# Optimization experiments

Hardware: AMD Instinct MI355X
Metric: run time of the kernel (lower is better)

## Reference

```python
import jax, jax.numpy as jnp
import numpy as np

R_MAX = 5.0
P_CUT = 5
NAVG = 16.0
L_OF_LM = np.array([0, 1, 1, 1, 2, 2, 2, 2, 2, 3, 3, 3, 3, 3, 3, 3])


def _sph(v):
    # real spherical harmonics up to l=3 on normalized vectors, [E,16]
    n = jnp.sqrt(jnp.sum(v * v, -1, keepdims=True) + 1e-12)
    u = v / n
    x, y, z = u[..., 0], u[..., 1], u[..., 2]
    s3, s15, s5 = np.sqrt(3.0), np.sqrt(15.0), np.sqrt(5.0)
    s70, s105, s42, s7 = np.sqrt(70.0), np.sqrt(105.0), np.sqrt(42.0), np.sqrt(7.0)
    Y = [jnp.ones_like(x),
         s3 * x, s3 * y, s3 * z,
         s15 * x * y, s15 * y * z, 0.5 * s5 * (3 * z * z - 1.0), s15 * x * z, 0.5 * s15 * (x * x - y * y),
         0.25 * s70 * y * (3 * x * x - y * y), s105 * x * y * z, 0.25 * s42 * y * (5 * z * z - 1.0),
         0.5 * s7 * z * (5 * z * z - 3.0), 0.25 * s42 * x * (5 * z * z - 1.0),
         0.5 * s105 * z * (x * x - y * y), 0.25 * s70 * x * (3 * x * x - y * y)]
    return jnp.stack(Y, -1)


def _radial(r):
    # Bessel basis * smooth polynomial cutoff, r: [E] -> [E, 8]
    n = jnp.arange(1, 9, dtype=r.dtype)
    bess = np.sqrt(2.0 / R_MAX) * jnp.sin(n * np.pi * r[:, None] / R_MAX) / (r[:, None] + 1e-9)
    u = r / R_MAX
    p = float(P_CUT)
    f = 1.0 - 0.5 * (p + 1) * (p + 2) * u ** P_CUT + p * (p + 2) * u ** (P_CUT + 1) - 0.5 * p * (p + 1) * u ** (P_CUT + 2)
    f = jnp.where(u < 1.0, f, 0.0)
    return bess * f[:, None]


def _energy(node_attrs, positions, shifts, atomic_energies, W_embed, W_up, W_r1, W_r2, W_r3,
            W_lin, W_skip, U1, U2, U3, Wc1, Wc2, Wc3, W_prod, W_readout,
            edge_index, batch, num_graphs):
    send, recv = edge_index[0], edge_index[1]
    vec = positions[recv] - positions[send] + shifts
    r = jnp.sqrt(jnp.sum(vec * vec, -1) + 1e-12)
    Y = _sph(vec)                       # [E,16]
    edge_feats = _radial(r)             # [E,8]
    h = node_attrs @ W_embed            # [N,K] scalar node features
    lidx = jnp.asarray(L_OF_LM)
    N = h.shape[0]
    for i in range(2):
        h_up = h @ W_up[i]
        w = jax.nn.silu(edge_feats @ W_r1[i])
        w = jax.nn.silu(w @ W_r2[i])
        w = (w @ W_r3[i]).reshape(edge_feats.shape[0], -1, 4)   # [E,K,4] per-l radial tp weights
        w_lm = w[:, :, lidx]                                    # [E,K,16]
        m = w_lm * h_up[send][:, :, None] * Y[:, None, :]       # scalar x SH tensor product messages
        agg = jax.ops.segment_sum(m, recv, num_segments=N) / NAVG
        Wm = W_lin[i][lidx]                                     # [16,K,K] per-l linear
        mixed = jnp.einsum('nkm,mkh->nhm', agg, Wm)
        sc = jnp.einsum('nk,ne,ekh->nh', h, node_attrs, W_skip[i])  # element-wise skip tp -> scalars
        A = mixed.at[:, :, 0].add(sc)                           # [N,K,16] A-basis
        # ACE symmetric product basis (invariant outputs), element-dependent weights
        w1 = jnp.einsum('ne,epk->npk', node_attrs, Wc1[i])
        b1 = jnp.einsum('nkp,npk->nk', jnp.einsum('nka,ap->nkp', A, U1), w1)
        AA = jnp.einsum('nka,nkb->nkab', A, A)                  # [N,K,16,16]
        w2 = jnp.einsum('ne,epk->npk', node_attrs, Wc2[i])
        b2 = jnp.einsum('nkp,npk->nk', jnp.einsum('nkab,abp->nkp', AA, U2), w2)
        T3 = jnp.einsum('nkab,abcp->nkcp', AA, U3)              # [N,K,16,8]
        w3 = jnp.einsum('ne,epk->npk', node_attrs, Wc3[i])
        b3 = jnp.einsum('nkp,npk->nk', jnp.einsum('nkcp,nkc->nkp', T3, A), w3)
        h = (b1 + b2 + b3) @ W_prod[i]
    node_es = h @ W_readout                                     # [N]
    node_e0 = node_attrs @ atomic_energies
    e0 = jax.ops.segment_sum(node_e0, batch, num_segments=num_graphs)
    inter = jax.ops.segment_sum(node_es, batch, num_segments=num_graphs)
    return e0 + inter


def setup_inputs():
    key = jax.random.key(0)
    ks = jax.random.split(key, 24)
    N, E, K, NE, G, NB = 2048, 32768, 128, 10, 16, 8
    P1, P2, P3, L = 2, 4, 8, 16

    def rn(k, shape, fan):
        return jax.random.normal(k, shape, jnp.float32) / np.sqrt(fan)

    elem = jax.random.randint(ks[0], (N,), 0, NE)
    return {
        'node_attrs': jax.nn.one_hot(elem, NE, dtype=jnp.float32),
        'positions': jax.random.uniform(ks[1], (N, 3), jnp.float32) * 6.0,
        'shifts': jnp.zeros((E, 3), jnp.float32),
        'atomic_energies': jax.random.normal(ks[2], (NE,), jnp.float32),
        'W_embed': rn(ks[3], (NE, K), NE),
        'W_up': rn(ks[4], (2, K, K), K),
        'W_r1': rn(ks[5], (2, NB, 64), NB),
        'W_r2': rn(ks[6], (2, 64, 64), 64),
        'W_r3': rn(ks[7], (2, 64, K * 4), 64),
        'W_lin': rn(ks[8], (2, 4, K, K), K),
        'W_skip': rn(ks[9], (2, NE, K, K), K),
        'U1': rn(ks[10], (L, P1), L),
        'U2': rn(ks[11], (L, L, P2), L * L),
        'U3': rn(ks[12], (L, L, L, P3), L * L * L),
        'Wc1': rn(ks[13], (2, NE, P1, K), P1),
        'Wc2': rn(ks[14], (2, NE, P2, K), P2),
        'Wc3': rn(ks[15], (2, NE, P3, K), P3),
        'W_prod': rn(ks[16], (2, K, K), K),
        'W_readout': rn(ks[17], (K,), K),
        'edge_index': jax.random.randint(ks[18], (2, E), 0, N).astype(jnp.int32),
        'batch': jnp.sort(jax.random.randint(ks[19], (N,), 0, G)).astype(jnp.int32),
        'num_graphs': 16,
    }


def reference(node_attrs, positions, shifts, atomic_energies, W_embed, W_up, W_r1, W_r2, W_r3,
              W_lin, W_skip, U1, U2, U3, Wc1, Wc2, Wc3, W_prod, W_readout,
              edge_index, batch, num_graphs):
    e_fn = lambda pos: _energy(node_attrs, pos, shifts, atomic_energies, W_embed, W_up, W_r1, W_r2,
                               W_r3, W_lin, W_skip, U1, U2, U3, Wc1, Wc2, Wc3, W_prod, W_readout,
                               edge_index, batch, num_graphs)
    energy = e_fn(positions)
    forces = -jax.grad(lambda p: e_fn(p).sum())(positions)
    return energy, forces
```

## Files before the change

### kernel.cpp

```cpp
#include <hip/hip_runtime.h>
#include <math.h>

#define KCH 128
#define NELEM 10
#define NPAIR 136
#define PSZ   2176

__device__ __forceinline__ int lidxf(int m){ return (m==0)?0:((m<4)?1:((m<9)?2:3)); }
__device__ __forceinline__ float siluf(float z){ return z/(1.f+expf(-z)); }
__device__ __forceinline__ float dsiluf(float z){ float s=1.f/(1.f+expf(-z)); return s*(1.f+z*(1.f-s)); }

__global__ void k_zero(float* p, int n){
  int i = blockIdx.x*256 + threadIdx.x;
  if(i<n) p[i]=0.f;
}

__global__ void k_elem(const float* attrs, int* elem, int N){
  int n = blockIdx.x*256 + threadIdx.x;
  if(n>=N) return;
  int z=0;
  for(int e=0;e<NELEM;++e) if(attrs[n*NELEM+e] > 0.5f) z=e;
  elem[n]=z;
}

// ... 209 lines not shown
  int e0 = blockIdx.x*16;
  for(int it=0; it<4; ++it){
    int item = t + it*256;
    int el = item>>6, j = item&63;
    float z=0;
    if(e0+el < E){
      const float* efe = ef + (size_t)(e0+el)*8;
      #pragma unroll
      for(int b=0;b<8;++b) z += efe[b]*Wr1[b*64+j];
    }
    t1s[el][j] = siluf(z);
  }
  __syncthreads();
  for(int it=0; it<4; ++it){
    int item = t + it*256;
    int el = item>>6, j = item&63;
    float z=0;
    #pragma unroll
    for(int i=0;i<64;++i) z += t1s[el][i]*Wr2[i*64+j];
    t2s[el][j] = siluf(z);
  }
  __syncthreads();
  float a0[16], a1[16];
  #pragma unroll
  for(int el=0;el<16;++el){ a0[el]=0.f; a1[el]=0.f; }
  for(int j=0;j<64;++j){
    float wa = Wr3[j*512 + t];
    float wb = Wr3[j*512 + t + 256];
    #pragma unroll
    for(int el=0;el<16;++el){
      float tv = t2s[el][j];
      a0[el] += tv*wa;
      a1[el] += tv*wb;
    }
  }
  for(int el=0;el<16;++el){
    if(e0+el < E){
      w[(size_t)(e0+el)*512 + t] = a0[el];
      w[(size_t)(e0+el)*512 + t + 256] = a1[el];
    }
  }
}

__global__ __launch_bounds__(256) void k_gather(const float* hup, const float* w, const float* Y,
                                                const int* rptr, const int* snds,
                                                float* agg, int E){
  int n = blockIdx.x;
  int t = threadIdx.x;
  int k = t & 127, mg = t >> 7;
  float acc[8] = {0,0,0,0,0,0,0,0};
  int s0 = rptr[n], s1 = rptr[n+1];
  for(int i=s0;i<s1;++i){
    int snd = snds[i];
    float hv = hup[(size_t)snd*KCH + k];
    float4 w4 = ((const float4*)(w + (size_t)i*512))[k];
    const float* Ye = Y + (size_t)i*16 + mg*8;
    if(mg==0){
      acc[0] += w4.x*hv*Ye[0];
      acc[1] += w4.y*hv*Ye[1];
      acc[2] += w4.y*hv*Ye[2];
      acc[3] += w4.y*hv*Ye[3];
      acc[4] += w4.z*hv*Ye[4];
      acc[5] += w4.z*hv*Ye[5];
      acc[6] += w4.z*hv*Ye[6];
      acc[7] += w4.z*hv*Ye[7];
    } else {
      acc[0] += w4.z*hv*Ye[0];
      acc[1] += w4.w*hv*Ye[1];
      acc[2] += w4.w*hv*Ye[2];
      acc[3] += w4.w*hv*Ye[3];
      acc[4] += w4.w*hv*Ye[4];
      acc[5] += w4.w*hv*Ye[5];
      acc[6] += w4.w*hv*Ye[6];
      acc[7] += w4.w*hv*Ye[7];
    }
  }
  const float inv = 1.f/16.f;
  float* ap = agg + (size_t)n*2048 + k*16 + mg*8;
  #pragma unroll
  for(int j=0;j<8;++j) ap[j] = acc[j]*inv;
}

__global__ __launch_bounds__(256) void k_mixed2(const float* X, const float* hin, const int* elem,
                                                const float* Wb, const float* Wsk,
                                                float* Out, float* gh, int N, int mode){
  __shared__ float xs[4][2048];
  __shared__ float hs[4][128];
  __shared__ int zs[4];
  int t = threadIdx.x;
  int n0 = blockIdx.x*4;
  for(int q=0;q<4;++q){
    const float4* Xp = (const float4*)(X + (size_t)(n0+q)*2048);
    float4* Xs = (float4*)xs[q];
    Xs[t] = Xp[t]; Xs[t+256] = Xp[t+256];
  }
  if(mode==0 && t<128){
    for(int q=0;q<4;++q) hs[q][t] = hin[(size_t)(n0+q)*KCH + t];
  }
  if(t<4) zs[t]=elem[n0+t];
  __syncthreads();
  int kg = t&31, mg=(t>>5)&3, half=t>>7;
  int k0 = kg*4, m0 = mg*4;
  int q0 = half*2, q1=q0+1;
  float acc0[4][4], acc1[4][4];
  #pragma unroll
  for(int a=0;a<4;++a){
    #pragma unroll
    for(int b=0;b<4;++b){acc0[a][b]=0.f;acc1[a][b]=0.f;}
  }
  for(int s=0;s<KCH;++s){
    float4 x0 = *(const float4*)&xs[q0][s*16+m0];
    float4 x1 = *(const float4*)&xs[q1][s*16+m0];
    #pragma unroll
    for(int mj=0;mj<4;++mj){
      const float4 wv = *(const float4*)&Wb[(size_t)(m0+mj)*16384 + s*128 + k0];
      float xm0 = (mj==0)?x0.x:((mj==1)?x0.y:((mj==2)?x0.z:x0.w));
      float xm1 = (mj==0)?x1.x:((mj==1)?x1.y:((mj==2)?x1.z:x1.w));
      acc0[mj][0]+=xm0*wv.x; acc0[mj][1]+=xm0*wv.y; acc0[mj][2]+=xm0*wv.z; acc0[mj][3]+=xm0*wv.w;
      acc1[mj][0]+=xm1*wv.x; acc1[mj][1]+=xm1*wv.y; acc1[mj][2]+=xm1*wv.z; acc1[mj][3]+=xm1*wv.w;
    }
  }
  if(mode==0 && mg==0){
    const float* W0 = Wsk + (size_t)zs[q0]*16384;
    const float* W1 = Wsk + (size_t)zs[q1]*16384;
    for(int s=0;s<KCH;++s){
      float h0v=hs[q0][s], h1v=hs[q1][s];
      float4 w0 = *(const float4*)&W0[s*128+k0];
      float4 w1 = *(const float4*)&W1[s*128+k0];
      acc0[0][0]+=h0v*w0.x; acc0[0][1]+=h0v*w0.y; acc0[0][2]+=h0v*w0.z; acc0[0][3]+=h0v*w0.w;
      acc1[0][0]+=h1v*w1.x; acc1[0][1]+=h1v*w1.y; acc1[0][2]+=h1v*w1.z; acc1[0][3]+=h1v*w1.w;
    }
  }
  #pragma unroll
  for(int ki=0;ki<4;++ki){
    *(float4*)&Out[(size_t)(n0+q0)*2048 + (k0+ki)*16 + m0] = make_float4(acc0[0][ki],acc0[1][ki],acc0[2][ki],acc0[3][ki]);
    *(float4*)&Out[(size_t)(n0+q1)*2048 + (k0+ki)*16 + m0] = make_float4(acc1[0][ki],acc1[1][ki],acc1[2][ki],acc1[3][ki]);
  }
  if(mode==2 && mg==0){
    const float* W0 = Wsk + (size_t)zs[q0]*16384;
    const float* W1 = Wsk + (size_t)zs[q1]*16384;
    float a0[4]={0,0,0,0}, a1[4]={0,0,0,0};
    for(int s=0;s<KCH;++s){
      float x0v = xs[q0][s*16], x1v = xs[q1][s*16];
      float4 w0 = *(const float4*)&W0[s*128+k0];
      float4 w1 = *(const float4*)&W1[s*128+k0];
      a0[0]+=x0v*w0.x; a0[1]+=x0v*w0.y; a0[2]+=x0v*w0.z; a0[3]+=x0v*w0.w;
      a1[0]+=x1v*w1.x; a1[1]+=x1v*w1.y; a1[2]+=x1v*w1.z; a1[3]+=x1v*w1.w;
    }
    *(float4*)&gh[(size_t)(n0+q0)*KCH + k0] = make_float4(a0[0],a0[1],a0[2],a0[3]);
    *(float4*)&gh[(size_t)(n0+q1)*KCH + k0] = make_float4(a1[0],a1[1],a1[2],a1[3]);
  }
}

__global__ __launch_bounds__(256) void k_poly_fwd(const float* A, const float* C1, const float* C2S, const float* P,
                                                  const int* eptr, const int* eidx, float* B){
  __shared__ float Ps[PSZ];
  __shared__ float C2s_[256];
  __shared__ float C1s_[16];
  int t = threadIdx.x;
  int z = blockIdx.x >> 7, c = blockIdx.x & 127;
  size_t cb = (size_t)z*KCH + c;
  for(int i=t;i<PSZ;i+=256) Ps[i] = P[cb*PSZ + i];
  if(t<256) C2s_[t] = C2S[cb*256 + t];
  if(t<16) C1s_[t] = C1[cb*16 + t];
  __syncthreads();
  int s0 = eptr[z], cnt = eptr[z+1]-s0;
  for(int idx=t; idx<cnt; idx+=256){
    int n = eidx[s0+idx];
    float a[16];
    const float4* ap = (const float4*)(A + (size_t)n*2048 + c*16);
    float4 a4;
    a4=ap[0]; a[0]=a4.x;a[1]=a4.y;a[2]=a4.z;a[3]=a4.w;
    a4=ap[1]; a[4]=a4.x;a[5]=a4.y;a[6]=a4.z;a[7]=a4.w;
    a4=ap[2]; a[8]=a4.x;a[9]=a4.y;a[10]=a4.z;a[11]=a4.w;
    a4=ap[3]; a[12]=a4.x;a[13]=a4.y;a[14]=a4.z;a[15]=a4.w;
    float G[16];
    #pragma unroll
    for(int x=0;x<16;++x) G[x]=0.f;
    int pair=0;
    #pragma unroll
    for(int j=0;j<16;++j){
      #pragma unroll
      for(int k=j;k<16;++k){
        float pp = a[j]*a[k];
        const float* Pp = &Ps[pair*16];
        #pragma unroll
        for(int x=0;x<16;++x) G[x] += pp*Pp[x];
        ++pair;
      }
    }
    float b1=0;
    #pragma unroll
    for(int i=0;i<16;++i) b1 += a[i]*C1s_[i];
    float b2=0;
    for(int i=0;i<16;++i){
      float s=0;
      #pragma unroll
      for(int j=0;j<16;++j) s += a[j]*C2s_[i*16+j];
      b2 += a[i]*s;
    }
    float b3o=0;
    #pragma unroll
    for(int x=0;x<16;++x) b3o += a[x]*G[x];
    B[(size_t)n*KCH + c] = b1 + 0.5f*b2 + b3o*(1.f/3.f);
  }
}

__global__ __launch_bounds__(256) void k_poly_bwd(const float* A, const float* C1, const float* C2S, const float* P,
                                                  const int* eptr, const int* eidx,
                                                  const float* gBvec, const float* gBbuf, float* gA){
  __shared__ float Ps[PSZ];
  __shared__ float C2s_[256];
  __shared__ float C1s_[16];
  int t = threadIdx.x;
  int z = blockIdx.x >> 7, c = blockIdx.x & 127;
  size_t cb = (size_t)z*KCH + c;
  for(int i=t;i<PSZ;i+=256) Ps[i] = P[cb*PSZ + i];
  if(t<256) C2s_[t] = C2S[cb*256 + t];
  if(t<16) C1s_[t] = C1[cb*16 + t];
  __syncthreads();
  int s0 = eptr[z], cnt = eptr[z+1]-s0;
  for(int idx=t; idx<cnt; idx+=256){
    int n = eidx[s0+idx];
    float a[16];
    const float4* ap = (const float4*)(A + (size_t)n*2048 + c*16);
    float4 a4;
    a4=ap[0]; a[0]=a4.x;a[1]=a4.y;a[2]=a4.z;a[3]=a4.w;
    a4=ap[1]; a[4]=a4.x;a[5]=a4.y;a[6]=a4.z;a[7]=a4.w;
    a4=ap[2]; a[8]=a4.x;a[9]=a4.y;a[10]=a4.z;a[11]=a4.w;
    a4=ap[3]; a[12]=a4.x;a[13]=a4.y;a[14]=a4.z;a[15]=a4.w;
    float gB = gBvec ? gBvec[c] : gBbuf[(size_t)n*KCH + c];
    float G[16];
    #pragma unroll
    for(int x=0;x<16;++x) G[x]=C1s_[x];
    for(int x=0;x<16;++x){
      float s=0;
      #pragma unroll
      for(int b=0;b<16;++b) s += a[b]*C2s_[x*16+b];
      G[x]+=s;
    }
    int pair=0;
    #pragma unroll
    for(int j=0;j<16;++j){
      #pragma unroll
      for(int k=j;k<16;++k){
        float pp = a[j]*a[k];
        const float* Pp = &Ps[pair*16];
        #pragma unroll
        for(int x=0;x<16;++x) G[x] += pp*Pp[x];
        ++pair;
      }
    }
    float* gp = gA + (size_t)n*2048 + c*16;
    #pragma unroll
    for(int x=0;x<16;++x) gp[x] = gB*G[x];
  }
}

__global__ __launch_bounds__(256) void k_edge_gw(const float* gagg, const float* hup, const float* w,
                                                 const float* Y, const float* dY,
                                                 const int* snds, const int* rcvs, int E,
                                                 float* gw, float* ghup, float* gvec, int do_ghup, int accv){
  __shared__ float Ys[2][16];
  __shared__ float gYp[2][2][16];
  int t = threadIdx.x;
  int le = t>>7, k = t&127;
  int e = blockIdx.x*2 + le;
  const float inv16 = 1.f/16.f;
  if(t<32){ int l2=t>>4; int ec=blockIdx.x*2+l2; if(ec<E) Ys[l2][t&15] = Y[(size_t)ec*16 + (t&15)]; }
  __syncthreads();
  bool valid = (e<E);
  int eC = valid ? e : (E-1);
  int snd = snds[eC], rcv = rcvs[eC];
  float hv = hup[(size_t)snd*KCH + k];
  float4 w4 = ((const float4*)(w + (size_t)eC*512))[k];
  float g[16];
  const float4* gp = (const float4*)(gagg + (size_t)rcv*2048 + k*16);
  float4 v4;
  v4=gp[0]; g[0]=v4.x;g[1]=v4.y;g[2]=v4.z;g[3]=v4.w;
  v4=gp[1]; g[4]=v4.x;g[5]=v4.y;g[6]=v4.z;g[7]=v4.w;
  v4=gp[2]; g[8]=v4.x;g[9]=v4.y;g[10]=v4.z;g[11]=v4.w;
  v4=gp[3]; g[12]=v4.x;g[13]=v4.y;g[14]=v4.z;g[15]=v4.w;
  const float* Yl = Ys[le];
  float p0 = g[0]*Yl[0];
  float p1 = g[1]*Yl[1]+g[2]*Yl[2]+g[3]*Yl[3];
  float p2 = g[4]*Yl[4]+g[5]*Yl[5]+g[6]*Yl[6]+g[7]*Yl[7]+g[8]*Yl[8];
  float p3 = g[9]*Yl[9]+g[10]*Yl[10]+g[11]*Yl[11]+g[12]*Yl[12]+g[13]*Yl[13]+g[14]*Yl[14]+g[15]*Yl[15];
  float hs = hv*inv16;
  ((float4*)(gw + (size_t)eC*512))[k] = make_float4(p0*hs, p1*hs, p2*hs, p3*hs);
  if(do_ghup && valid){
    float s = (p0*w4.x + p1*w4.y + p2*w4.z + p3*w4.w)*inv16;
    atomicAdd(&ghup[(size_t)snd*KCH+k], s);
  }
  float q[16];
  q[0]=g[0]*w4.x*hv;
  q[1]=g[1]*w4.y*hv; q[2]=g[2]*w4.y*hv; q[3]=g[3]*w4.y*hv;
  q[4]=g[4]*w4.z*hv; q[5]=g[5]*w4.z*hv; q[6]=g[6]*w4.z*hv; q[7]=g[7]*w4.z*hv; q[8]=g[8]*w4.z*hv;
  #pragma unroll
  for(int m=9;m<16;++m) q[m]=g[m]*w4.w*hv;
  #pragma unroll
  for(int m=0;m<16;++m){
    float vv=q[m];
    #pragma unroll
    for(int off2=1; off2<64; off2<<=1) vv += __shfl_xor(vv, off2, 64);
    q[m]=vv;
  }
  if((t&63)==0){
    int wv2 = (t>>6)&1;
    #pragma unroll
    for(int m=0;m<16;++m) gYp[le][wv2][m]=q[m];
  }
  __syncthreads();
  if(t<6){
    int le2 = t/3, jj = t-le2*3;
    int ee = blockIdx.x*2 + le2;
    if(ee<E){
      float s=0;
      #pragma unroll
      for(int m=0;m<16;++m)
        s += (gYp[le2][0][m]+gYp[le2][1][m])*inv16 * dY[(size_t)ee*48 + m*3 + jj];
      if(accv) gvec[(size_t)ee*3+jj] += s;
      else     gvec[(size_t)ee*3+jj]  = s;
    }
  }
}

__global__ __launch_bounds__(256) void k_radial_bwd2(const float* gw, const float* ef, const float* defdr,
                                                     const float* vec, const float* rr,
                                                     const float* Wr1, const float* Wr2,
                                                     const float* Wr2T, const float* Wr3T,
                                                     float* gvec, int E){
  __shared__ float t1s[16][64];
  __shared__ float gz2s[16][64];
  __shared__ float efS[16][8];
  __shared__ float defS[16][8];
  int t = threadIdx.x;
  int e0 = blockIdx.x*16;
  int j = t&63, g = t>>6;
  if(t<128){ int el=t>>3, b=t&7; int ec=e0+el;
    if(ec<E){ efS[el][b]=ef[(size_t)ec*8+b]; defS[el][b]=defdr[(size_t)ec*8+b]; }
    else { efS[el][b]=0.f; defS[el][b]=0.f; } }
  __syncthreads();
  float ds1[4], ds2[4];
  #pragma unroll
  for(int q=0;q<4;++q){
    int el = g*4+q;
    float z=0;
    #pragma unroll
    for(int b=0;b<8;++b) z += efS[el][b]*Wr1[b*64+j];
    t1s[el][j]=siluf(z); ds1[q]=dsiluf(z);
  }
  __syncthreads();
  float gt2[4]={0,0,0,0};
  #pragma unroll
  for(int q=0;q<4;++q){
    int el = g*4+q;
    float z=0;
    for(int i=0;i<64;++i) z += t1s[el][i]*Wr2[i*64+j];
    ds2[q]=dsiluf(z);
  }
  for(int i4=0;i4<128;++i4){
    float wv0 = Wr3T[(i4*4+0)*64+j];
    float wv1 = Wr3T[(i4*4+1)*64+j];
    float wv2 = Wr3T[(i4*4+2)*64+j];
    float wv3 = Wr3T[(i4*4+3)*64+j];
    #pragma unroll
    for(int q=0;q<4;++q){
      int ec = e0 + g*4 + q; if(ec>=E) ec=E-1;
      const float4 g4 = *(const float4*)(gw + (size_t)ec*512 + i4*4);
      gt2[q] += g4.x*wv0 + g4.y*wv1 + g4.z*wv2 + g4.w*wv3;
    }
  }
  #pragma unroll
  for(int q=0;q<4;++q) gz2s[g*4+q][j] = gt2[q]*ds2[q];
  __syncthreads();
  #pragma unroll
  for(int q=0;q<4;++q){
    int el = g*4+q;
    float s=0;
    for(int o=0;o<64;++o) s += gz2s[el][o]*Wr2T[o*64+j];
    float gz1 = s*ds1[q];
    float cj=0;
    #pragma unroll
    for(int b=0;b<8;++b) cj += Wr1[b*64+j]*defS[el][b];
    float p = gz1*cj;
    #pragma unroll
    for(int off2=1;off2<64;off2<<=1) p += __shfl_xor(p,off2,64);
    int ec = e0+el;
    if(j<3 && ec<E)
      gvec[(size_t)ec*3+j] += p * vec[(size_t)ec*3+j] / rr[ec];
  }
}

__global__ __launch_bounds__(256) void k_edge_bwd2(const float* gagg, const float* hup, const float* w,
                                                   const float* Y, const float* dY,
                                                   const float* vec, const float* rr,
                                                   const float* ef, const float* defdr,
                                                   const float* Wr1, const float* Wr2,
                                                   const float* Wr2T, const float* Wr3T,
                                                   const int* snds, const int* rcvs, int E,
                                                   float* ghup, float* gvec, int do_ghup, int accv){
  __shared__ float Ys[4][16];
  __shared__ float gwS[4][512];
  __shared__ float gYp[4][2][16];
  __shared__ float t1s[4][64];
  __shared__ float gz2s[4][64];
  __shared__ float efS[4][8];
  __shared__ float defS[4][8];
  int t = threadIdx.x;
  int e0 = blockIdx.x*4;
  const float inv16 = 1.f/16.f;
  if(t<64){ int le=t>>4; int ec = e0+le; if(ec<E) Ys[le][t&15] = Y[(size_t)ec*16 + (t&15)]; }
  else if(t<96){ int i=t-64; int le=i>>3; int ec=e0+le; if(ec<E) efS[le][i&7]=ef[(size_t)ec*8+(i&7)]; }
  else if(t<128){ int i=t-96; int le=i>>3; int ec=e0+le; if(ec<E) defS[le][i&7]=defdr[(size_t)ec*8+(i&7)]; }
  __syncthreads();
  for(int rep=0;rep<2;++rep){
    int le = (t>>7) + 2*rep;
    int k = t&127;
    int e = e0+le;
    bool valid = (e<E);
    int eC = valid ? e : (E-1);
    int snd = snds[eC], rcv = rcvs[eC];
    float hv = hup[(size_t)snd*KCH + k];
    float4 w4 = ((const float4*)(w + (size_t)eC*512))[k];
    float g[16];
    const float4* gp = (const float4*)(gagg + (size_t)rcv*2048 + k*16);
    float4 v4;
    v4=gp[0]; g[0]=v4.x;g[1]=v4.y;g[2]=v4.z;g[3]=v4.w;
    v4=gp[1]; g[4]=v4.x;g[5]=v4.y;g[6]=v4.z;g[7]=v4.w;
    v4=gp[2]; g[8]=v4.x;g[9]=v4.y;g[10]=v4.z;g[11]=v4.w;
    v4=gp[3]; g[12]=v4.x;g[13]=v4.y;g[14]=v4.z;g[15]=v4.w;
    const float* Yl = Ys[le];
    float p0 = g[0]*Yl[0];
    float p1 = g[1]*Yl[1]+g[2]*Yl[2]+g[3]*Yl[3];
    float p2 = g[4]*Yl[4]+g[5]*Yl[5]+g[6]*Yl[6]+g[7]*Yl[7]+g[8]*Yl[8];
    float p3 = g[9]*Yl[9]+g[10]*Yl[10]+g[11]*Yl[11]+g[12]*Yl[12]+g[13]*Yl[13]+g[14]*Yl[14]+g[15]*Yl[15];
    float hs = hv*inv16;
    ((float4*)(&gwS[le][k*4]))[0] = make_float4(p0*hs, p1*hs, p2*hs, p3*hs);
    if(do_ghup && valid){
      float s = (p0*w4.x + p1*w4.y + p2*w4.z + p3*w4.w)*inv16;
      atomicAdd(&ghup[(size_t)snd*KCH+k], s);
    }
    float q[16];
    q[0]=g[0]*w4.x*hv;
    q[1]=g[1]*w4.y*hv; q[2]=g[2]*w4.y*hv; q[3]=g[3]*w4.y*hv;
    q[4]=g[4]*w4.z*hv; q[5]=g[5]*w4.z*hv; q[6]=g[6]*w4.z*hv; q[7]=g[7]*w4.z*hv; q[8]=g[8]*w4.z*hv;
    #pragma unroll
    for(int m=9;m<16;++m) q[m]=g[m]*w4.w*hv;
    #pragma unroll
    for(int m=0;m<16;++m){
      float vv=q[m];
      #pragma unroll
      for(int off2=1; off2<64; off2<<=1) vv += __shfl_xor(vv, off2, 64);
      q[m]=vv;
    }
    if((t&63)==0){
      int wv2 = (t>>6)&1;
      #pragma unroll
      for(int m=0;m<16;++m) gYp[le][wv2][m]=q[m];
    }
  }
  __syncthreads();
  {
    int el = t>>6, j = t&63;
    int e = e0+el;
    bool valid = (e<E);
    int eC = valid ? e : (E-1);
    float z1=0;
    #pragma unroll
    for(int b=0;b<8;++b) z1 += efS[el][b]*Wr1[b*64+j];
    float ds1v = dsiluf(z1);
    t1s[el][j] = siluf(z1);
    __syncthreads();
    float z2=0;
    for(int i=0;i<64;++i) z2 += t1s[el][i]*Wr2[i*64+j];
    float ds2v = dsiluf(z2);
    float gt2=0;
    for(int i=0;i<512;++i) gt2 += gwS[el][i]*Wr3T[i*64+j];
    gz2s[el][j] = gt2*ds2v;
    __syncthreads();
    float gz1=0;
    for(int o=0;o<64;++o) gz1 += gz2s[el][o]*Wr2T[o*64+j];
    gz1 *= ds1v;
    float cj=0;
    #pragma unroll
    for(int b=0;b<8;++b) cj += Wr1[b*64+j]*defS[el][b];
    float p = gz1*cj;
    #pragma unroll
    for(int off2=1;off2<64;off2<<=1) p += __shfl_xor(p,off2,64);
    if(j<3 && valid){
      float s = p * vec[(size_t)eC*3+j] / rr[eC];
      #pragma unroll
      for(int m=0;m<16;++m)
        s += (gYp[el][0][m]+gYp[el][1][m])*inv16 * dY[(size_t)eC*48 + m*3 + j];
      if(accv) gvec[(size_t)eC*3+j] += s;
      else     gvec[(size_t)eC*3+j]  = s;
    }
  }
}

__global__ void k_energy(const float* h2, const float* Wro, const float* AE,
                         const int* elem, const int* batch, float* out, int N){
  int n = blockIdx.x*256 + threadIdx.x;
  if(n>=N) return;
  float s=0;
  for(int k=0;k<KCH;++k) s += h2[(size_t)n*KCH+k]*Wro[k];
  s += AE[elem[n]];
  atomicAdd(&out[batch[n]], s);
}

__global__ void k_forces(const float* gvec, const int* snds, const int* rcvs, int E, float* fout){
  int i = blockIdx.x*256 + threadIdx.x;
  if(i>=E*3) return;
  int e = i/3, j = i - e*3;
  float g = gvec[i];
  atomicAdd(&fout[(size_t)snds[e]*3+j], g);
  atomicAdd(&fout[(size_t)rcvs[e]*3+j], -g);
}

extern "C" void kernel_launch(void* const* d_in, const int* in_sizes, int n_in,
                              void* d_out, int out_size, void* d_ws, size_t ws_size,
                              hipStream_t stream){
  const float* attrs  = (const float*)d_in[0];
  const float* pos    = (const float*)d_in[1];
  const float* shifts = (const float*)d_in[2];
  const float* AE     = (const float*)d_in[3];
  const float* Wemb   = (const float*)d_in[4];
  const float* Wup    = (const float*)d_in[5];
  const float* Wr1    = (const float*)d_in[6];
  const float* Wr2    = (const float*)d_in[7];
  const float* Wr3    = (const float*)d_in[8];
  const float* Wlin   = (const float*)d_in[9];
  const float* Wskip  = (const float*)d_in[10];
  const float* U1     = (const float*)d_in[11];
  const float* U2     = (const float*)d_in[12];
  const float* U3     = (const float*)d_in[13];
  const float* Wc1    = (const float*)d_in[14];
  const float* Wc2    = (const float*)d_in[15];
  const float* Wc3    = (const float*)d_in[16];
  const float* Wprod  = (const float*)d_in[17];
  const float* Wro    = (const float*)d_in[18];
  const int*   ei     = (const int*)d_in[19];
  const int*   batch  = (const int*)d_in[20];
  int N = in_sizes[1]/3;
  int E = in_sizes[19]/2;
  float* out = (float*)d_out;
  int G = out_size - 3*N;

  char* base = (char*)d_ws;
  size_t off = 0;
  auto alloc = [&](size_t nbytes)->void*{
    void* p = base + off;
    off += (nbytes + 255) & ~(size_t)255;
    return p;
  };
  int* elem = (int*)alloc((size_t)N*4);
  int* rptr = (int*)alloc((size_t)(N+1)*4);
  int* rcnt = (int*)alloc((size_t)N*4);
  int* rcur = (int*)alloc((size_t)N*4);
  int* ecnt = (int*)alloc((size_t)NELEM*4);
  int* ecur = (int*)alloc((size_t)NELEM*4);
  size_t zspan = (size_t)((base+off) - (char*)rcnt) / 4;
  int* ridx = (int*)alloc((size_t)E*4);
  int* eptr = (int*)alloc((size_t)(NELEM+1)*4);
  int* eidx = (int*)alloc((size_t)N*4);
  int* snds = (int*)alloc((size_t)E*4);
  int* rcvs = (int*)alloc((size_t)E*4);
  float* h0   = (float*)alloc((size_t)N*KCH*4);
  float* h1   = (float*)alloc((size_t)N*KCH*4);
  float* h2   = (float*)alloc((size_t)N*KCH*4);
  float* hup0 = (float*)alloc((size_t)N*KCH*4);
  float* hup1 = (float*)alloc((size_t)N*KCH*4);
  float* vecb = (float*)alloc((size_t)E*3*4);
  float* rb   = (float*)alloc((size_t)E*4);
  float* Yb   = (float*)alloc((size_t)E*16*4);
  float* dYb  = (float*)alloc((size_t)E*48*4);
  float* efb  = (float*)alloc((size_t)E*8*4);
  float* defb = (float*)alloc((size_t)E*8*4);
  float* wb   = (float*)alloc((size_t)E*512*4);
  float* A0   = (float*)alloc((size_t)N*2048*4);
  float* A1   = (float*)alloc((size_t)N*2048*4);
  float* aggb = (float*)alloc((size_t)N*2048*4);
  float* gAb  = (float*)alloc((size_t)N*2048*4);
  float* Bbuf = (float*)alloc((size_t)N*KCH*4);
  float* gh1  = (float*)alloc((size_t)N*KCH*4);
  float* ghup = (float*)alloc((size_t)N*KCH*4);
  float* gB0b = (float*)alloc((size_t)N*KCH*4);
  float* gB1v = (float*)alloc((size_t)KCH*4);
  float* gvecb= (float*)alloc((size_t)E*3*4);
  float* C1b  = (float*)alloc((size_t)NELEM*KCH*16*4);
  float* C2Sb = (float*)alloc((size_t)NELEM*KCH*256*4);
  float* Pb   = (float*)alloc((size_t)NELEM*KCH*PSZ*4);
  float* U2s  = (float*)alloc(1024*4);
  float* U3s  = (float*)alloc(32768*4);
  float* WupT1   = (float*)alloc(16384*4);
  float* WprodT0 = (float*)alloc(16384*4);
  float* WskipT1 = (float*)alloc((size_t)NELEM*16384*4);
  float* Wbig0  = (float*)alloc((size_t)16*16384*4);
  float* Wbig1  = (float*)alloc((size_t)16*16384*4);
  float* WbigT0 = (float*)alloc((size_t)16*16384*4);
  float* WbigT1 = (float*)alloc((size_t)16*16384*4);
  float* Wr3T0   = (float*)alloc(32768*4);
  float* Wr3T1   = (float*)alloc(32768*4);
  float* Wr2T0   = (float*)alloc(4096*4);
  float* Wr2T1   = (float*)alloc(4096*4);
  if(off > ws_size) return;
  float* wb1 = wb; int have_wb1 = 0;
  if(off + (size_t)E*512*4 <= ws_size){ wb1 = (float*)alloc((size_t)E*512*4); have_wb1 = 1; }
  float *C1_1=C1b, *C2_1=C2Sb, *P_1=Pb; int have_c2 = 0;
  {
    size_t need = ((size_t)NELEM*KCH*16 + (size_t)NELEM*KCH*256 + (size_t)NELEM*KCH*PSZ)*4 + 1024;
    if(off + need <= ws_size){
      C1_1 = (float*)alloc((size_t)NELEM*KCH*16*4);
      C2_1 = (float*)alloc((size_t)NELEM*KCH*256*4);
      P_1  = (float*)alloc((size_t)NELEM*KCH*PSZ*4);
      have_c2 = 1;
    }
  }
  float* gwb = nullptr; int have_gw = 0;
  if(off + (size_t)E*512*4 <= ws_size){ gwb = (float*)alloc((size_t)E*512*4); have_gw = 1; }

  const int KK = KCH*KCH;
  dim3 b256(256), b128(128);
  #define GR(n) dim3(((n)+255)/256)

  k_zero<<<GR(out_size),b256,0,stream>>>(out, out_size);
  k_zero<<<GR((int)zspan),b256,0,stream>>>((float*)rcnt, (int)zspan);
  k_zero<<<GR(N*KCH),b256,0,stream>>>(ghup, N*KCH);

  k_elem<<<GR(N),b256,0,stream>>>(attrs, elem, N);
  k_h0<<<GR(N*KCH),b256,0,stream>>>(Wemb, elem, h0, N);

  k_hist<<<GR(E),b256,0,stream>>>(ei+E, rcnt, E);
  k_scan<<<1,b256,0,stream>>>(rcnt, rptr, N);
  k_scatter<<<GR(E),b256,0,stream>>>(ei+E, rptr, rcur, ridx, E);
  k_hist<<<GR(N),b256,0,stream>>>(elem, ecnt, N);
  k_scan<<<1,b256,0,stream>>>(ecnt, eptr, NELEM);
  k_scatter<<<GR(N),b256,0,stream>>>(elem, eptr, ecur, eidx, N);

  k_prep<<<GR(PREP_ITEMS),b256,0,stream>>>(Wup, Wprod, Wskip, Wlin, Wr2, Wr3, U2, U3,
                                           WupT1, WprodT0, WskipT1,
                                           Wbig0, Wbig1, WbigT0, WbigT1,
                                           Wr3T0, Wr3T1, Wr2T0, Wr2T1, U2s, U3s);
  k_gB1<<<1,b128,0,stream>>>(Wro, Wprod + KK, gB1v);

  k_edge_geom<<<GR(E),b256,0,stream>>>(pos, shifts, ei, ridx, E, snds, rcvs,
                                       vecb, rb, Yb, dYb, efb, defb);

  dim3 mmG((N+7)/8);
  dim3 mxG((N+3)/4);
  dim3 polyG(NELEM*KCH);
  dim3 rwG((E+15)/16);
  dim3 ebG((E+3)/4);
  dim3 egwG((E+1)/2);
  dim3 rbG((E+15)/16);

  k_ctens<<<GR(CTENS_ITEMS),b256,0,stream>>>(U1, U2s, U3s, Wc1, Wc2, Wc3, C1b, C2Sb, Pb);
  k_mm<<<mmG,b128,0,stream>>>(h0, Wup, hup0, N, 0);
  k_radial_w<<<rwG,b256,0,stream>>>(efb, Wr1, Wr2, Wr3, wb, E);
  k_gather<<<dim3(N),b256,0,stream>>>(hup0, wb, Yb, rptr, snds, aggb, E);
  k_mixed2<<<mxG,b256,0,stream>>>(aggb, h0, elem, Wbig0, Wskip, A0, nullptr, N, 0);
  k_poly_fwd<<<polyG,b256,0,stream>>>(A0, C1b, C2Sb, Pb, eptr, eidx, Bbuf);
  k_mm<<<mmG,b128,0,stream>>>(Bbuf, Wprod, h1, N, 0);

  k_ctens<<<GR(CTENS_ITEMS),b256,0,stream>>>(U1, U2s, U3s,
                                             Wc1 + NELEM*2*KCH, Wc2 + NELEM*4*KCH, Wc3 + NELEM*8*KCH,
                                             C1_1, C2_1, P_1);
  k_mm<<<mmG,b128,0,stream>>>(h1, Wup + KK, hup1, N, 0);
  k_radial_w<<<rwG,b256,0,stream>>>(efb, Wr1 + 512, Wr2 + 4096, Wr3 + 32768, wb1, E);
  k_gather<<<dim3(N),b256,0,stream>>>(hup1, wb1, Yb, rptr, snds, aggb, E);
  k_mixed2<<<mxG,b256,0,stream>>>(aggb, h1, elem, Wbig1, Wskip + (size_t)NELEM*KK, A1, nullptr, N, 0);
  k_poly_fwd<<<polyG,b256,0,stream>>>(A1, C1_1, C2_1, P_1, eptr, eidx, Bbuf);
  k_mm<<<mmG,b128,0,stream>>>(Bbuf, Wprod + KK, h2, N, 0);

  k_energy<<<GR(N),b256,0,stream>>>(h2, Wro, AE, elem, batch, out, N);

  k_poly_bwd<<<polyG,b256,0,stream>>>(A1, C1_1, C2_1, P_1, eptr, eidx, gB1v, nullptr, gAb);
  k_mixed2<<<mxG,b256,0,stream>>>(gAb, nullptr, elem, WbigT1, WskipT1, aggb, gh1, N, 2);
  if(have_gw){
    k_edge_gw<<<egwG,b256,0,stream>>>(aggb, hup1, wb1, Yb, dYb, snds, rcvs, E,
                                      gwb, ghup, gvecb, 1, 0);
    k_radial_bwd2<<<rbG,b256,0,stream>>>(gwb, efb, defb, vecb, rb,
                                         Wr1 + 512, Wr2 + 4096, Wr2T1, Wr3T1, gvecb, E);
  } else {
    k_edge_bwd2<<<ebG,b256,0,stream>>>(aggb, hup1, wb1, Yb, dYb, vecb, rb, efb, defb,
                                       Wr1 + 512, Wr2 + 4096, Wr2T1, Wr3T1, snds, rcvs, E,
                                       ghup, gvecb, 1, 0);
  }
  k_mm<<<mmG,b128,0,stream>>>(ghup, WupT1, gh1, N, 1);

  if(!have_c2)
    k_ctens<<<GR(CTENS_ITEMS),b256,0,stream>>>(U1, U2s, U3s, Wc1, Wc2, Wc3, C1b, C2Sb, Pb);
  k_mm<<<mmG,b128,0,stream>>>(gh1, WprodT0, gB0b, N, 0);
  k_poly_bwd<<<polyG,b256,0,stream>>>(A0, C1b, C2Sb, Pb, eptr, eidx, nullptr, gB0b, gAb);
  k_mixed2<<<mxG,b256,0,stream>>>(gAb, nullptr, elem, WbigT0, nullptr, aggb, nullptr, N, 1);
  if(!have_wb1)
    k_radial_w<<<rwG,b256,0,stream>>>(efb, Wr1, Wr2, Wr3, wb, E);
  if(have_gw){
    k_edge_gw<<<egwG,b256,0,stream>>>(aggb, hup0, wb, Yb, dYb, snds, rcvs, E,
                                      gwb, ghup, gvecb, 0, 1);
    k_radial_bwd2<<<rbG,b256,0,stream>>>(gwb, efb, defb, vecb, rb,
                                         Wr1, Wr2, Wr2T0, Wr3T0, gvecb, E);
  } else {
    k_edge_bwd2<<<ebG,b256,0,stream>>>(aggb, hup0, wb, Yb, dYb, vecb, rb, efb, defb,
                                       Wr1, Wr2, Wr2T0, Wr3T0, snds, rcvs, E,
                                       ghup, gvecb, 0, 1);
  }

  k_forces<<<GR(E*3),b256,0,stream>>>(gvecb, snds, rcvs, E, out + G);
  #undef GR
}
```

Baseline: 1.895 ms.

## Fuse polynomial forward/backward into one kernel, two nodes per thread, drop gw path

```diff
diff --git a/kernel.cpp b/kernel.cpp
--- a/kernel.cpp
+++ b/kernel.cpp
@@ -385,243 +385,97 @@
   }
 }
 
-__global__ __launch_bounds__(256) void k_poly_fwd(const float* A, const float* C1, const float* C2S, const float* P,
-                                                  const int* eptr, const int* eidx, float* B){
+__global__ __launch_bounds__(128) void k_poly(const float* A, const float* C1, const float* C2S, const float* P,
+                                              const int* eptr, const int* eidx,
+                                              float* B, float* gA,
+                                              const float* gBvec, const float* gBbuf){
   __shared__ float Ps[PSZ];
   __shared__ float C2s_[256];
   __shared__ float C1s_[16];
   int t = threadIdx.x;
   int z = blockIdx.x >> 7, c = blockIdx.x & 127;
   size_t cb = (size_t)z*KCH + c;
-  for(int i=t;i<PSZ;i+=256) Ps[i] = P[cb*PSZ + i];
-  if(t<256) C2s_[t] = C2S[cb*256 + t];
-  if(t<16) C1s_[t] = C1[cb*16 + t];
+  {
+    const float4* Pg = (const float4*)(P + cb*PSZ);
+    float4* Ps4 = (float4*)Ps;
+    for(int i=t;i<PSZ/4;i+=128) Ps4[i] = Pg[i];
+    const float4* Cg = (const float4*)(C2S + cb*256);
+    float4* Cs4 = (float4*)C2s_;
+    if(t<64) Cs4[t] = Cg[t];
+    if(t<16) C1s_[t] = C1[cb*16 + t];
+  }
   __syncthreads();
   int s0 = eptr[z], cnt = eptr[z+1]-s0;
-  for(int idx=t; idx<cnt; idx+=256){
-    int n = eidx[s0+idx];
-    float a[16];
-    const float4* ap = (const float4*)(A + (size_t)n*2048 + c*16);
-    float4 a4;
-    a4=ap[0]; a[0]=a4.x;a[1]=a4.y;a[2]=a4.z;a[3]=a4.w;
-    a4=ap[1]; a[4]=a4.x;a[5]=a4.y;a[6]=a4.z;a[7]=a4.w;
-    a4=ap[2]; a[8]=a4.x;a[9]=a4.y;a[10]=a4.z;a[11]=a4.w;
-    a4=ap[3]; a[12]=a4.x;a[13]=a4.y;a[14]=a4.z;a[15]=a4.w;
-    float G[16];
-    #pragma unroll
-    for(int x=0;x<16;++x) G[x]=0.f;
+  int half = (cnt+1)>>1;
+  for(int idx=t; idx<half; idx+=128){
+    int n0 = eidx[s0+idx];
+    bool has1 = (idx+half < cnt);
+    int n1 = has1 ? eidx[s0+idx+half] : n0;
+    float a0[16], a1[16], G0[16], G1[16];
+    {
+      const float4* ap = (const float4*)(A + (size_t)n0*2048 + c*16);
+      float4 v;
+      v=ap[0]; a0[0]=v.x;a0[1]=v.y;a0[2]=v.z;a0[3]=v.w;
+      v=ap[1]; a0[4]=v.x;a0[5]=v.y;a0[6]=v.z;a0[7]=v.w;
+      v=ap[2]; a0[8]=v.x;a0[9]=v.y;a0[10]=v.z;a0[11]=v.w;
+      v=ap[3]; a0[12]=v.x;a0[13]=v.y;a0[14]=v.z;a0[15]=v.w;
+      const float4* bp = (const float4*)(A + (size_t)n1*2048 + c*16);
+      v=bp[0]; a1[0]=v.x;a1[1]=v.y;a1[2]=v.z;a1[3]=v.w;
+      v=bp[1]; a1[4]=v.x;a1[5]=v.y;a1[6]=v.z;a1[7]=v.w;
+      v=bp[2]; a1[8]=v.x;a1[9]=v.y;a1[10]=v.z;a1[11]=v.w;
+      v=bp[3]; a1[12]=v.x;a1[13]=v.y;a1[14]=v.z;a1[15]=v.w;
+    }
+    float b1_0=0.f, b1_1=0.f, b2_0=0.f, b2_1=0.f;
+    #pragma unroll
+    for(int x=0;x<16;++x){
+      float cv0=0.f, cv1=0.f;
+      #pragma unroll
+      for(int b=0;b<16;++b){
+        float wv = C2s_[x*16+b];
+        cv0 += a0[b]*wv; cv1 += a1[b]*wv;
+      }
+      float c1v = C1s_[x];
+      G0[x] = c1v + cv0;  G1[x] = c1v + cv1;
+      b1_0 += a0[x]*c1v;  b1_1 += a1[x]*c1v;
+      b2_0 += a0[x]*cv0;  b2_1 += a1[x]*cv1;
+    }
     int pair=0;
     #pragma unroll
     for(int j=0;j<16;++j){
       #pragma unroll
       for(int k=j;k<16;++k){
-        float pp = a[j]*a[k];
-        const float* Pp = &Ps[pair*16];
+        float pp0 = a0[j]*a0[k];
+        float pp1 = a1[j]*a1[k];
+        const float4* Pp = (const float4*)&Ps[pair*16];
         #pragma unroll
-        for(int x=0;x<16;++x) G[x] += pp*Pp[x];
+        for(int q4=0;q4<4;++q4){
+          float4 pv = Pp[q4];
+          G0[q4*4+0] += pp0*pv.x; G0[q4*4+1] += pp0*pv.y; G0[q4*4+2] += pp0*pv.z; G0[q4*4+3] += pp0*pv.w;
+          G1[q4*4+0] += pp1*pv.x; G1[q4*4+1] += pp1*pv.y; G1[q4*4+2] += pp1*pv.z; G1[q4*4+3] += pp1*pv.w;
+        }
         ++pair;
       }
     }
-    float b1=0;
-    #pragma unroll
-    for(int i=0;i<16;++i) b1 += a[i]*C1s_[i];
-    float b2=0;
-    for(int i=0;i<16;++i){
-      float s=0;
+    if(B){
+      float d0=0.f, d1=0.f;
       #pragma unroll
-      for(int j=0;j<16;++j) s += a[j]*C2s_[i*16+j];
-      b2 += a[i]*s;
-    }
-    float b3o=0;
-    #pragma unroll
-    for(int x=0;x<16;++x) b3o += a[x]*G[x];
-    B[(size_t)n*KCH + c] = b1 + 0.5f*b2 + b3o*(1.f/3.f);
-  }
-}
-
-__global__ __launch_bounds__(256) void k_poly_bwd(const float* A, const float* C1, const float* C2S, const float* P,
-                                                  const int* eptr, const int* eidx,
-                                                  const float* gBvec, const float* gBbuf, float* gA){
-  __shared__ float Ps[PSZ];
-  __shared__ float C2s_[256];
-  __shared__ float C1s_[16];
-  int t = threadIdx.x;
-  int z = blockIdx.x >> 7, c = blockIdx.x & 127;
-  size_t cb = (size_t)z*KCH + c;
-  for(int i=t;i<PSZ;i+=256) Ps[i] = P[cb*PSZ + i];
-  if(t<256) C2s_[t] = C2S[cb*256 + t];
-  if(t<16) C1s_[t] = C1[cb*16 + t];
-  __syncthreads();
-  int s0 = eptr[z], cnt = eptr[z+1]-s0;
-  for(int idx=t; idx<cnt; idx+=256){
-    int n = eidx[s0+idx];
-    float a[16];
-    const float4* ap = (const float4*)(A + (size_t)n*2048 + c*16);
-    float4 a4;
-    a4=ap[0]; a[0]=a4.x;a[1]=a4.y;a[2]=a4.z;a[3]=a4.w;
-    a4=ap[1]; a[4]=a4.x;a[5]=a4.y;a[6]=a4.z;a[7]=a4.w;
-    a4=ap[2]; a[8]=a4.x;a[9]=a4.y;a[10]=a4.z;a[11]=a4.w;
-    a4=ap[3]; a[12]=a4.x;a[13]=a4.y;a[14]=a4.z;a[15]=a4.w;
-    float gB = gBvec ? gBvec[c] : gBbuf[(size_t)n*KCH + c];
-    float G[16];
-    #pragma unroll
-    for(int x=0;x<16;++x) G[x]=C1s_[x];
-    for(int x=0;x<16;++x){
-      float s=0;
+      for(int x=0;x<16;++x){ d0 += a0[x]*G0[x]; d1 += a1[x]*G1[x]; }
+      B[(size_t)n0*KCH + c] = (2.f/3.f)*b1_0 + (1.f/6.f)*b2_0 + (1.f/3.f)*d0;
+      if(has1)
+        B[(size_t)n1*KCH + c] = (2.f/3.f)*b1_1 + (1.f/6.f)*b2_1 + (1.f/3.f)*d1;
+    }
+    if(gA){
+      float g0 = gBvec ? gBvec[c] : gBbuf[(size_t)n0*KCH + c];
+      float* gp0 = gA + (size_t)n0*2048 + c*16;
       #pragma unroll
-      for(int b=0;b<16;++b) s += a[b]*C2s_[x*16+b];
-      G[x]+=s;
-    }
-    int pair=0;
-    #pragma unroll
-    for(int j=0;j<16;++j){
-      #pragma unroll
-      for(int k=j;k<16;++k){
-        float pp = a[j]*a[k];
-        const float* Pp = &Ps[pair*16];
+      for(int x=0;x<16;++x) gp0[x] = g0*G0[x];
+      if(has1){
+        float g1 = gBvec ? gBvec[c] : gBbuf[(size_t)n1*KCH + c];
+        float* gp1 = gA + (size_t)n1*2048 + c*16;
         #pragma unroll
-        for(int x=0;x<16;++x) G[x] += pp*Pp[x];
-        ++pair;
+        for(int x=0;x<16;++x) gp1[x] = g1*G1[x];
       }
     }
-    float* gp = gA + (size_t)n*2048 + c*16;
-    #pragma unroll
-    for(int x=0;x<16;++x) gp[x] = gB*G[x];
-  }
-}
-
-__global__ __launch_bounds__(256) void k_edge_gw(const float* gagg, const float* hup, const float* w,
-                                                 const float* Y, const float* dY,
-                                                 const int* snds, const int* rcvs, int E,
-                                                 float* gw, float* ghup, float* gvec, int do_ghup, int accv){
-  __shared__ float Ys[2][16];
-  __shared__ float gYp[2][2][16];
-  int t = threadIdx.x;
-  int le = t>>7, k = t&127;
-  int e = blockIdx.x*2 + le;
-  const float inv16 = 1.f/16.f;
-  if(t<32){ int l2=t>>4; int ec=blockIdx.x*2+l2; if(ec<E) Ys[l2][t&15] = Y[(size_t)ec*16 + (t&15)]; }
-  __syncthreads();
-  bool valid = (e<E);
-  int eC = valid ? e : (E-1);
-  int snd = snds[eC], rcv = rcvs[eC];
-  float hv = hup[(size_t)snd*KCH + k];
-  float4 w4 = ((const float4*)(w + (size_t)eC*512))[k];
-  float g[16];
-  const float4* gp = (const float4*)(gagg + (size_t)rcv*2048 + k*16);
-  float4 v4;
-  v4=gp[0]; g[0]=v4.x;g[1]=v4.y;g[2]=v4.z;g[3]=v4.w;
-  v4=gp[1]; g[4]=v4.x;g[5]=v4.y;g[6]=v4.z;g[7]=v4.w;
-  v4=gp[2]; g[8]=v4.x;g[9]=v4.y;g[10]=v4.z;g[11]=v4.w;
-  v4=gp[3]; g[12]=v4.x;g[13]=v4.y;g[14]=v4.z;g[15]=v4.w;
-  const float* Yl = Ys[le];
-  float p0 = g[0]*Yl[0];
-  float p1 = g[1]*Yl[1]+g[2]*Yl[2]+g[3]*Yl[3];
-  float p2 = g[4]*Yl[4]+g[5]*Yl[5]+g[6]*Yl[6]+g[7]*Yl[7]+g[8]*Yl[8];
-  float p3 = g[9]*Yl[9]+g[10]*Yl[10]+g[11]*Yl[11]+g[12]*Yl[12]+g[13]*Yl[13]+g[14]*Yl[14]+g[15]*Yl[15];
-  float hs = hv*inv16;
-  ((float4*)(gw + (size_t)eC*512))[k] = make_float4(p0*hs, p1*hs, p2*hs, p3*hs);
-  if(do_ghup && valid){
-    float s = (p0*w4.x + p1*w4.y + p2*w4.z + p3*w4.w)*inv16;
-    atomicAdd(&ghup[(size_t)snd*KCH+k], s);
-  }
-  float q[16];
-  q[0]=g[0]*w4.x*hv;
-  q[1]=g[1]*w4.y*hv; q[2]=g[2]*w4.y*hv; q[3]=g[3]*w4.y*hv;
-  q[4]=g[4]*w4.z*hv; q[5]=g[5]*w4.z*hv; q[6]=g[6]*w4.z*hv; q[7]=g[7]*w4.z*hv; q[8]=g[8]*w4.z*hv;
-  #pragma unroll
-  for(int m=9;m<16;++m) q[m]=g[m]*w4.w*hv;
-  #pragma unroll
-  for(int m=0;m<16;++m){
-    float vv=q[m];
-    #pragma unroll
-    for(int off2=1; off2<64; off2<<=1) vv += __shfl_xor(vv, off2, 64);
-    q[m]=vv;
-  }
-  if((t&63)==0){
-    int wv2 = (t>>6)&1;
-    #pragma unroll
-    for(int m=0;m<16;++m) gYp[le][wv2][m]=q[m];
-  }
-  __syncthreads();
-  if(t<6){
-    int le2 = t/3, jj = t-le2*3;
-    int ee = blockIdx.x*2 + le2;
-    if(ee<E){
-      float s=0;
-      #pragma unroll
-      for(int m=0;m<16;++m)
-        s += (gYp[le2][0][m]+gYp[le2][1][m])*inv16 * dY[(size_t)ee*48 + m*3 + jj];
-      if(accv) gvec[(size_t)ee*3+jj] += s;
-      else     gvec[(size_t)ee*3+jj]  = s;
-    }
-  }
-}
-
-__global__ __launch_bounds__(256) void k_radial_bwd2(const float* gw, const float* ef, const float* defdr,
-                                                     const float* vec, const float* rr,
-                                                     const float* Wr1, const float* Wr2,
-                                                     const float* Wr2T, const float* Wr3T,
-                                                     float* gvec, int E){
-  __shared__ float t1s[16][64];
-  __shared__ float gz2s[16][64];
-  __shared__ float efS[16][8];
-  __shared__ float defS[16][8];
-  int t = threadIdx.x;
-  int e0 = blockIdx.x*16;
-  int j = t&63, g = t>>6;
-  if(t<128){ int el=t>>3, b=t&7; int ec=e0+el;
-    if(ec<E){ efS[el][b]=ef[(size_t)ec*8+b]; defS[el][b]=defdr[(size_t)ec*8+b]; }
-    else { efS[el][b]=0.f; defS[el][b]=0.f; } }
-  __syncthreads();
-  float ds1[4], ds2[4];
-  #pragma unroll
-  for(int q=0;q<4;++q){
-    int el = g*4+q;
-    float z=0;
-    #pragma unroll
-    for(int b=0;b<8;++b) z += efS[el][b]*Wr1[b*64+j];
-    t1s[el][j]=siluf(z); ds1[q]=dsiluf(z);
-  }
-  __syncthreads();
-  float gt2[4]={0,0,0,0};
-  #pragma unroll
-  for(int q=0;q<4;++q){
-    int el = g*4+q;
-    float z=0;
-    for(int i=0;i<64;++i) z += t1s[el][i]*Wr2[i*64+j];
-    ds2[q]=dsiluf(z);
-  }
-  for(int i4=0;i4<128;++i4){
-    float wv0 = Wr3T[(i4*4+0)*64+j];
-    float wv1 = Wr3T[(i4*4+1)*64+j];
-    float wv2 = Wr3T[(i4*4+2)*64+j];
-    float wv3 = Wr3T[(i4*4+3)*64+j];
-    #pragma unroll
-    for(int q=0;q<4;++q){
-      int ec = e0 + g*4 + q; if(ec>=E) ec=E-1;
-      const float4 g4 = *(const float4*)(gw + (size_t)ec*512 + i4*4);
-      gt2[q] += g4.x*wv0 + g4.y*wv1 + g4.z*wv2 + g4.w*wv3;
-    }
-  }
-  #pragma unroll
-  for(int q=0;q<4;++q) gz2s[g*4+q][j] = gt2[q]*ds2[q];
-  __syncthreads();
-  #pragma unroll
-  for(int q=0;q<4;++q){
-    int el = g*4+q;
-    float s=0;
-    for(int o=0;o<64;++o) s += gz2s[el][o]*Wr2T[o*64+j];
-    float gz1 = s*ds1[q];
-    float cj=0;
-    #pragma unroll
-    for(int b=0;b<8;++b) cj += Wr1[b*64+j]*defS[el][b];
-    float p = gz1*cj;
-    #pragma unroll
-    for(int off2=1;off2<64;off2<<=1) p += __shfl_xor(p,off2,64);
-    int ec = e0+el;
-    if(j<3 && ec<E)
-      gvec[(size_t)ec*3+j] += p * vec[(size_t)ec*3+j] / rr[ec];
   }
 }
 
@@ -838,8 +692,7 @@
   float* Wr2T0   = (float*)alloc(4096*4);
   float* Wr2T1   = (float*)alloc(4096*4);
   if(off > ws_size) return;
-  float* wb1 = wb; int have_wb1 = 0;
-  if(off + (size_t)E*512*4 <= ws_size){ wb1 = (float*)alloc((size_t)E*512*4); have_wb1 = 1; }
+
   float *C1_1=C1b, *C2_1=C2Sb, *P_1=Pb; int have_c2 = 0;
   {
     size_t need = ((size_t)NELEM*KCH*16 + (size_t)NELEM*KCH*256 + (size_t)NELEM*KCH*PSZ)*4 + 1024;
@@ -850,8 +703,8 @@
       have_c2 = 1;
     }
   }
-  float* gwb = nullptr; int have_gw = 0;
-  if(off + (size_t)E*512*4 <= ws_size){ gwb = (float*)alloc((size_t)E*512*4); have_gw = 1; }
+  float* wb1 = wb; int have_wb1 = 0;
+  if(off + (size_t)E*512*4 <= ws_size){ wb1 = (float*)alloc((size_t)E*512*4); have_wb1 = 1; }
 
   const int KK = KCH*KCH;
   dim3 b256(256), b128(128);
@@ -885,15 +738,13 @@
   dim3 polyG(NELEM*KCH);
   dim3 rwG((E+15)/16);
   dim3 ebG((E+3)/4);
-  dim3 egwG((E+1)/2);
-  dim3 rbG((E+15)/16);
 
   k_ctens<<<GR(CTENS_ITEMS),b256,0,stream>>>(U1, U2s, U3s, Wc1, Wc2, Wc3, C1b, C2Sb, Pb);
   k_mm<<<mmG,b128,0,stream>>>(h0, Wup, hup0, N, 0);
   k_radial_w<<<rwG,b256,0,stream>>>(efb, Wr1, Wr2, Wr3, wb, E);
   k_gather<<<dim3(N),b256,0,stream>>>(hup0, wb, Yb, rptr, snds, aggb, E);
   k_mixed2<<<mxG,b256,0,stream>>>(aggb, h0, elem, Wbig0, Wskip, A0, nullptr, N, 0);
-  k_poly_fwd<<<polyG,b256,0,stream>>>(A0, C1b, C2Sb, Pb, eptr, eidx, Bbuf);
+  k_poly<<<polyG,b128,0,stream>>>(A0, C1b, C2Sb, Pb, eptr, eidx, Bbuf, nullptr, nullptr, nullptr);
   k_mm<<<mmG,b128,0,stream>>>(Bbuf, Wprod, h1, N, 0);
 
   k_ctens<<<GR(CTENS_ITEMS),b256,0,stream>>>(U1, U2s, U3s,
@@ -903,42 +754,27 @@
   k_radial_w<<<rwG,b256,0,stream>>>(efb, Wr1 + 512, Wr2 + 4096, Wr3 + 32768, wb1, E);
   k_gather<<<dim3(N),b256,0,stream>>>(hup1, wb1, Yb, rptr, snds, aggb, E);
   k_mixed2<<<mxG,b256,0,stream>>>(aggb, h1, elem, Wbig1, Wskip + (size_t)NELEM*KK, A1, nullptr, N, 0);
-  k_poly_fwd<<<polyG,b256,0,stream>>>(A1, C1_1, C2_1, P_1, eptr, eidx, Bbuf);
+  k_poly<<<polyG,b128,0,stream>>>(A1, C1_1, C2_1, P_1, eptr, eidx, Bbuf, gAb, gB1v, nullptr);
   k_mm<<<mmG,b128,0,stream>>>(Bbuf, Wprod + KK, h2, N, 0);
 
   k_energy<<<GR(N),b256,0,stream>>>(h2, Wro, AE, elem, batch, out, N);
 
-  k_poly_bwd<<<polyG,b256,0,stream>>>(A1, C1_1, C2_1, P_1, eptr, eidx, gB1v, nullptr, gAb);
   k_mixed2<<<mxG,b256,0,stream>>>(gAb, nullptr, elem, WbigT1, WskipT1, aggb, gh1, N, 2);
-  if(have_gw){
-    k_edge_gw<<<egwG,b256,0,stream>>>(aggb, hup1, wb1, Yb, dYb, snds, rcvs, E,
-                                      gwb, ghup, gvecb, 1, 0);
-    k_radial_bwd2<<<rbG,b256,0,stream>>>(gwb, efb, defb, vecb, rb,
-                                         Wr1 + 512, Wr2 + 4096, Wr2T1, Wr3T1, gvecb, E);
-  } else {
-    k_edge_bwd2<<<ebG,b256,0,stream>>>(aggb, hup1, wb1, Yb, dYb, vecb, rb, efb, defb,
-                                       Wr1 + 512, Wr2 + 4096, Wr2T1, Wr3T1, snds, rcvs, E,
-                                       ghup, gvecb, 1, 0);
-  }
+  k_edge_bwd2<<<ebG,b256,0,stream>>>(aggb, hup1, wb1, Yb, dYb, vecb, rb, efb, defb,
+                                     Wr1 + 512, Wr2 + 4096, Wr2T1, Wr3T1, snds, rcvs, E,
+                                     ghup, gvecb, 1, 0);
   k_mm<<<mmG,b128,0,stream>>>(ghup, WupT1, gh1, N, 1);
 
   if(!have_c2)
     k_ctens<<<GR(CTENS_ITEMS),b256,0,stream>>>(U1, U2s, U3s, Wc1, Wc2, Wc3, C1b, C2Sb, Pb);
   k_mm<<<mmG,b128,0,stream>>>(gh1, WprodT0, gB0b, N, 0);
-  k_poly_bwd<<<polyG,b256,0,stream>>>(A0, C1b, C2Sb, Pb, eptr, eidx, nullptr, gB0b, gAb);
+  k_poly<<<polyG,b128,0,stream>>>(A0, C1b, C2Sb, Pb, eptr, eidx, nullptr, gAb, nullptr, gB0b);
   k_mixed2<<<mxG,b256,0,stream>>>(gAb, nullptr, elem, WbigT0, nullptr, aggb, nullptr, N, 1);
   if(!have_wb1)
     k_radial_w<<<rwG,b256,0,stream>>>(efb, Wr1, Wr2, Wr3, wb, E);
-  if(have_gw){
-    k_edge_gw<<<egwG,b256,0,stream>>>(aggb, hup0, wb, Yb, dYb, snds, rcvs, E,
-                                      gwb, ghup, gvecb, 0, 1);
-    k_radial_bwd2<<<rbG,b256,0,stream>>>(gwb, efb, defb, vecb, rb,
-                                         Wr1, Wr2, Wr2T0, Wr3T0, gvecb, E);
-  } else {
-    k_edge_bwd2<<<ebG,b256,0,stream>>>(aggb, hup0, wb, Yb, dYb, vecb, rb, efb, defb,
-                                       Wr1, Wr2, Wr2T0, Wr3T0, snds, rcvs, E,
-                                       ghup, gvecb, 0, 1);
-  }
+  k_edge_bwd2<<<ebG,b256,0,stream>>>(aggb, hup0, wb, Yb, dYb, vecb, rb, efb, defb,
+                                     Wr1, Wr2, Wr2T0, Wr3T0, snds, rcvs, E,
+                                     ghup, gvecb, 0, 1);
 
   k_forces<<<GR(E*3),b256,0,stream>>>(gvecb, snds, rcvs, E, out + G);
   #undef GR
```

New measurement: 1.717 ms. 1.1x faster.
